# Optimization experiments

Measured on AMD Instinct MI355X. Metric: run time of the kernel, lower is better.

## Reference

```python
import jax, jax.numpy as jnp
import numpy as np

RES = 0.1


def setup_inputs() -> dict:
    key = jax.random.key(0)
    k1, k2 = jax.random.split(key)
    B, N, H, W = 512, 8192, 200, 200
    # positions in [-11, 11] so some points land out of the valid [-9.9, 9.9] range
    opState = jax.random.uniform(k1, (B, N, 2), dtype=jnp.float32, minval=-11.0, maxval=11.0)
    # ESDF distances in [0, 2) meters
    envs = jax.random.uniform(k2, (B, 1, H, W), dtype=jnp.float32) * 2.0
    return {"opState": opState, "envs": envs}


def reference(opState, envs):
    # opState: [B, N, 2] world positions; envs: [B, 1, 200, 200] ESDF map
    out_range = jnp.any((opState < -9.9) | (opState > 9.9), axis=-1)  # [B, N]
    pos = jnp.clip(opState, -9.9, 9.9)
    pos_m = pos - 0.5 * RES
    idx = jnp.floor((pos_m + 10.0) / RES).astype(jnp.int32)           # [B, N, 2]
    idx_pos = (idx.astype(jnp.float32) + 0.5) * RES - 10.0
    diff = (pos - idx_pos) / RES                                       # [B, N, 2]

    esdf = envs[:, 0]                                                  # [B, H, W]
    b = jnp.arange(esdf.shape[0])[:, None]                             # [B, 1]
    ix, iy = idx[..., 0], idx[..., 1]
    # 4-corner gather for bilinear interpolation
    v00 = esdf[b, ix,     iy    ]
    v10 = esdf[b, ix + 1, iy    ]
    v01 = esdf[b, ix,     iy + 1]
    v11 = esdf[b, ix + 1, iy + 1]

    dx, dy = diff[..., 0], diff[..., 1]
    vx0 = (1.0 - dx) * v00 + dx * v10
    vx1 = (1.0 - dx) * v01 + dx * v11
    v = (1.0 - dy) * vx0 + dy * vx1
    dists = jnp.where(out_range, -1.0, v)                              # [B, N]

    viod = 10.0 * (0.3 - dists)
    penalty = jnp.square(jax.nn.relu(viod))  # positiveSmoothedL2
    return jnp.mean(penalty)
```

## Files before the change

### kernel.cpp

```cpp
#include <hip/hip_runtime.h>

#define RES 0.1f

constexpr int B_ = 512;
constexpr int N_ = 8192;
constexpr int H_ = 200;
constexpr int W_ = 200;
constexpr int MAP = H_ * W_;
constexpr long long TOTAL = (long long)B_ * N_;

constexpr int TPB = 1024;

__global__ __launch_bounds__(TPB) void collision_lds(
    const float* __restrict__ opState,
    const float* __restrict__ envs,
    float* __restrict__ partial)
{
    __shared__ float smap[MAP];
    const int b   = blockIdx.x;
    const int tid = threadIdx.x;

    {
        const float4* m4 = (const float4*)(envs + (long long)b * MAP);
        float4* s4 = (float4*)smap;
        #pragma unroll
        for (int j = tid; j < MAP / 4; j += TPB)
            s4[j] = m4[j];
    }
    __syncthreads();

    const float2* pts = (const float2*)opState + (long long)b * N_;
    float acc = 0.0f;

    #pragma unroll
    for (int k = 0; k < N_ / TPB; ++k) {
        const int n = tid + k * TPB;
        float2 p = pts[n];

        bool out_range = (p.x < -9.9f) | (p.x > 9.9f) |
                         (p.y < -9.9f) | (p.y > 9.9f);

        float px = fminf(fmaxf(p.x, -9.9f), 9.9f);
        float py = fminf(fmaxf(p.y, -9.9f), 9.9f);

        float pmx = px - 0.5f * RES;
        float pmy = py - 0.5f * RES;

        int ix = (int)floorf((pmx + 10.0f) * 10.0f);
        int iy = (int)floorf((pmy + 10.0f) * 10.0f);

        float ipx = ((float)ix + 0.5f) * RES - 10.0f;
        float ipy = ((float)iy + 0.5f) * RES - 10.0f;

        float dx = (px - ipx) * 10.0f;
        float dy = (py - ipy) * 10.0f;

        int base = ix * W_ + iy;
        float v00 = smap[base];
        float v01 = smap[base + 1];
        float v10 = smap[base + W_];
        float v11 = smap[base + W_ + 1];

        float vx0 = (1.0f - dx) * v00 + dx * v10;
        float vx1 = (1.0f - dx) * v01 + dx * v11;
        float v   = (1.0f - dy) * vx0 + dy * vx1;

        float dists = out_range ? -1.0f : v;
        float viod  = 10.0f * (0.3f - dists);
        float r     = viod > 0.0f ? viod : 0.0f;
        acc += r * r;
    }

    #pragma unroll
    for (int off = 32; off > 0; off >>= 1)
        acc += __shfl_down(acc, off, 64);

    __shared__ float sacc[TPB / 64];
    const int lane = tid & 63;
    const int wid  = tid >> 6;
    if (lane == 0) sacc[wid] = acc;
    __syncthreads();

    if (tid == 0) {
        float s = 0.0f;
        #pragma unroll
        for (int w = 0; w < TPB / 64; ++w) s += sacc[w];
        partial[b] = s;
    }
}

__global__ __launch_bounds__(512) void collision_final(
    const float* __restrict__ partial,
    float* __restrict__ out)
{
    float acc = partial[threadIdx.x];

    #pragma unroll
    for (int off = 32; off > 0; off >>= 1)
        acc += __shfl_down(acc, off, 64);

    __shared__ float sacc[8];
    const int lane = threadIdx.x & 63;
    const int wid  = threadIdx.x >> 6;
    if (lane == 0) sacc[wid] = acc;
    __syncthreads();

    if (threadIdx.x == 0) {
        float s = 0.0f;
        #pragma unroll
        for (int w = 0; w < 8; ++w) s += sacc[w];
        out[0] = s / (float)TOTAL;
    }
}

extern "C" void kernel_launch(void* const* d_in, const int* in_sizes, int n_in,
                              void* d_out, int out_size, void* d_ws, size_t ws_size,
                              hipStream_t stream) {
    const float* opState = (const float*)d_in[0];
    const float* envs    = (const float*)d_in[1];
    float* out     = (float*)d_out;
    float* partial = (float*)d_ws;

    collision_lds<<<B_, TPB, 0, stream>>>(opState, envs, partial);
    collision_final<<<1, 512, 0, stream>>>(partial, out);
}
```

Baseline: 146.0 us.

## Store ESDF map as fp16 in LDS, prefetch points, fuse final reduction

Converts the per-batch ESDF map to half precision when staging into shared memory, halving LDS usage so more blocks can reside per CU. Point loads are issued as float4 before the map copy to overlap latency, and the second reduction kernel is replaced by a per-block atomicAdd after a memset. This trades interpolation precision (fp16 map values) and nondeterministic summation order for occupancy and fewer launches; the launch-bounds hint may also constrain registers.

```diff
diff --git a/kernel.cpp b/kernel.cpp
--- a/kernel.cpp
+++ b/kernel.cpp
@@ -1,81 +1,88 @@
 #include <hip/hip_runtime.h>
+#include <hip/hip_fp16.h>
 
 #define RES 0.1f
 
-constexpr int B_ = 512;
-constexpr int N_ = 8192;
-constexpr int H_ = 200;
-constexpr int W_ = 200;
-constexpr int MAP = H_ * W_;
+constexpr int B_  = 512;
+constexpr int N_  = 8192;
+constexpr int W_  = 200;
+constexpr int MAP = 200 * 200;
 constexpr long long TOTAL = (long long)B_ * N_;
 
 constexpr int TPB = 1024;
 
-__global__ __launch_bounds__(TPB) void collision_lds(
+__global__ __launch_bounds__(TPB, 8) void collision_fused(
     const float* __restrict__ opState,
     const float* __restrict__ envs,
-    float* __restrict__ partial)
+    float* __restrict__ out)
 {
-    __shared__ float smap[MAP];
+    __shared__ __half smap[MAP];
+    __shared__ float  sacc[TPB / 64];
+
     const int b   = blockIdx.x;
     const int tid = threadIdx.x;
 
-    {
-        const float4* m4 = (const float4*)(envs + (long long)b * MAP);
-        float4* s4 = (float4*)smap;
-        #pragma unroll
-        for (int j = tid; j < MAP / 4; j += TPB)
-            s4[j] = m4[j];
+    const float4* p4 = (const float4*)(opState + (long long)b * N_ * 2);
+    float4 pp0 = p4[tid];
+    float4 pp1 = p4[tid + TPB];
+    float4 pp2 = p4[tid + 2 * TPB];
+    float4 pp3 = p4[tid + 3 * TPB];
+
+    const float4* m4 = (const float4*)(envs + (long long)b * MAP);
+    #pragma unroll
+    for (int k = 0; k < 9; ++k) {
+        const int j = tid + k * TPB;
+        float4 v = m4[j];
+        __half2 h01 = __floats2half2_rn(v.x, v.y);
+        __half2 h23 = __floats2half2_rn(v.z, v.w);
+        *(__half2*)(smap + 4 * j)     = h01;
+        *(__half2*)(smap + 4 * j + 2) = h23;
+    }
+    if (tid < MAP / 4 - 9 * TPB) {
+        const int j = tid + 9 * TPB;
+        float4 v = m4[j];
+        __half2 h01 = __floats2half2_rn(v.x, v.y);
+        __half2 h23 = __floats2half2_rn(v.z, v.w);
+        *(__half2*)(smap + 4 * j)     = h01;
+        *(__half2*)(smap + 4 * j + 2) = h23;
     }
     __syncthreads();
 
-    const float2* pts = (const float2*)opState + (long long)b * N_;
     float acc = 0.0f;
-
-    #pragma unroll
-    for (int k = 0; k < N_ / TPB; ++k) {
-        const int n = tid + k * TPB;
-        float2 p = pts[n];
-
-        bool out_range = (p.x < -9.9f) | (p.x > 9.9f) |
-                         (p.y < -9.9f) | (p.y > 9.9f);
-
-        float px = fminf(fmaxf(p.x, -9.9f), 9.9f);
-        float py = fminf(fmaxf(p.y, -9.9f), 9.9f);
-
+    auto point = [&](float x, float y) {
+        bool oor = (x < -9.9f) | (x > 9.9f) | (y < -9.9f) | (y > 9.9f);
+        float px = fminf(fmaxf(x, -9.9f), 9.9f);
+        float py = fminf(fmaxf(y, -9.9f), 9.9f);
         float pmx = px - 0.5f * RES;
         float pmy = py - 0.5f * RES;
-
         int ix = (int)floorf((pmx + 10.0f) * 10.0f);
         int iy = (int)floorf((pmy + 10.0f) * 10.0f);
-
         float ipx = ((float)ix + 0.5f) * RES - 10.0f;
         float ipy = ((float)iy + 0.5f) * RES - 10.0f;
-
         float dx = (px - ipx) * 10.0f;
         float dy = (py - ipy) * 10.0f;
-
         int base = ix * W_ + iy;
-        float v00 = smap[base];
-        float v01 = smap[base + 1];
-        float v10 = smap[base + W_];
-        float v11 = smap[base + W_ + 1];
-
+        float v00 = __half2float(smap[base]);
+        float v01 = __half2float(smap[base + 1]);
+        float v10 = __half2float(smap[base + W_]);
+        float v11 = __half2float(smap[base + W_ + 1]);
         float vx0 = (1.0f - dx) * v00 + dx * v10;
         float vx1 = (1.0f - dx) * v01 + dx * v11;
         float v   = (1.0f - dy) * vx0 + dy * vx1;
-
-        float dists = out_range ? -1.0f : v;
+        float dists = oor ? -1.0f : v;
         float viod  = 10.0f * (0.3f - dists);
-        float r     = viod > 0.0f ? viod : 0.0f;
+        float r     = fmaxf(viod, 0.0f);
         acc += r * r;
-    }
+    };
+    point(pp0.x, pp0.y); point(pp0.z, pp0.w);
+    point(pp1.x, pp1.y); point(pp1.z, pp1.w);
+    point(pp2.x, pp2.y); point(pp2.z, pp2.w);
+    point(pp3.x, pp3.y); point(pp3.z, pp3.w);
 
     #pragma unroll
     for (int off = 32; off > 0; off >>= 1)
         acc += __shfl_down(acc, off, 64);
 
-    __shared__ float sacc[TPB / 64];
     const int lane = tid & 63;
     const int wid  = tid >> 6;
     if (lane == 0) sacc[wid] = acc;
@@ -85,31 +92,7 @@
         float s = 0.0f;
         #pragma unroll
         for (int w = 0; w < TPB / 64; ++w) s += sacc[w];
-        partial[b] = s;
-    }
-}
-
-__global__ __launch_bounds__(512) void collision_final(
-    const float* __restrict__ partial,
-    float* __restrict__ out)
-{
-    float acc = partial[threadIdx.x];
-
-    #pragma unroll
-    for (int off = 32; off > 0; off >>= 1)
-        acc += __shfl_down(acc, off, 64);
-
-    __shared__ float sacc[8];
-    const int lane = threadIdx.x & 63;
-    const int wid  = threadIdx.x >> 6;
-    if (lane == 0) sacc[wid] = acc;
-    __syncthreads();
-
-    if (threadIdx.x == 0) {
-        float s = 0.0f;
-        #pragma unroll
-        for (int w = 0; w < 8; ++w) s += sacc[w];
-        out[0] = s / (float)TOTAL;
+        atomicAdd(out, s * (1.0f / (float)TOTAL));
     }
 }
 
@@ -118,9 +101,8 @@
                               hipStream_t stream) {
     const float* opState = (const float*)d_in[0];
     const float* envs    = (const float*)d_in[1];
-    float* out     = (float*)d_out;
-    float* partial = (float*)d_ws;
+    float* out = (float*)d_out;
 
-    collision_lds<<<B_, TPB, 0, stream>>>(opState, envs, partial);
-    collision_final<<<1, 512, 0, stream>>>(partial, out);
+    hipMemsetAsync(out, 0, sizeof(float), stream);
+    collision_fused<<<B_, TPB, 0, stream>>>(opState, envs, out);
 }
```

Result: no change. 147.1 us (+0.7%).
